# Optimization experiments

Measured on AMD Instinct MI355X. Metric: run time of the kernel, lower is better.

The kernel has to match this reference:

```python
import jax, jax.numpy as jnp
import numpy as np

FEATURE_DIM = 128
HIDDEN_DIM = 64
MAPPING_SIZE = 64
SCALE = 10.0
B, N, H, W = 8, 65536, 56, 56


def setup_inputs() -> dict:
    key = jax.random.key(0)
    ks = jax.random.split(key, 12)
    features = jax.random.normal(ks[0], (B, FEATURE_DIM, H, W), dtype=jnp.float32)
    # points in [-1, 1]^3
    points = jax.random.uniform(ks[1], (B, N, 3), dtype=jnp.float32, minval=-1.0, maxval=1.0)
    # realistic pinhole intrinsics for a 56x56 feature map
    k_mat = jnp.array([[56.0, 0.0, 28.0], [0.0, 56.0, 28.0], [0.0, 0.0, 1.0]], dtype=jnp.float32)
    k = jnp.broadcast_to(k_mat, (B, 3, 3))
    # extrinsics: identity rotation, translate z by 2 so points are in front of camera
    rt_mat = jnp.concatenate([jnp.eye(3, dtype=jnp.float32), jnp.array([[0.0], [0.0], [2.0]], dtype=jnp.float32)], axis=1)
    rt = jnp.broadcast_to(rt_mat, (B, 3, 4))
    # learned params
    B_gauss = jax.random.normal(ks[2], (MAPPING_SIZE, 3), dtype=jnp.float32) * SCALE
    input_dim = FEATURE_DIM + 2 * MAPPING_SIZE
    W1 = jax.random.normal(ks[3], (input_dim, HIDDEN_DIM), dtype=jnp.float32) * 0.05
    b1 = jnp.zeros((HIDDEN_DIM,), dtype=jnp.float32)
    W2 = jax.random.normal(ks[4], (HIDDEN_DIM, HIDDEN_DIM), dtype=jnp.float32) * 0.05
    b2 = jnp.zeros((HIDDEN_DIM,), dtype=jnp.float32)
    W3 = jax.random.normal(ks[5], (HIDDEN_DIM, HIDDEN_DIM), dtype=jnp.float32) * 0.05
    b3 = jnp.zeros((HIDDEN_DIM,), dtype=jnp.float32)
    W4 = jax.random.normal(ks[6], (HIDDEN_DIM, 1), dtype=jnp.float32) * 0.05
    b4 = jnp.zeros((1,), dtype=jnp.float32)
    return {"features": features, "points": points, "k": k, "rt": rt,
            "B_gauss": B_gauss, "W1": W1, "b1": b1, "W2": W2, "b2": b2,
            "W3": W3, "b3": b3, "W4": W4, "b4": b4}


def _grid_sample_bilinear_zeros(grid, x, y):
    # grid: (B, C, H, W); x, y: (B, N) pixel coords (align_corners=False already unnormalized)
    Bc, C, Hc, Wc = grid.shape
    g = jnp.transpose(grid, (0, 2, 3, 1))  # (B, H, W, C)
    x0 = jnp.floor(x)
    y0 = jnp.floor(y)
    wx1 = x - x0  # frac
    wy1 = y - y0
    wx0 = 1.0 - wx1
    wy0 = 1.0 - wy1
    x0i = x0.astype(jnp.int32)
    y0i = y0.astype(jnp.int32)
    bidx = jnp.arange(Bc, dtype=jnp.int32)[:, None]  # (B, 1)

    def gather(ix, iy):
        inb = ((ix >= 0) & (ix < Wc) & (iy >= 0) & (iy < Hc)).astype(grid.dtype)  # (B, N)
        vals = g[bidx, jnp.clip(iy, 0, Hc - 1), jnp.clip(ix, 0, Wc - 1)]  # (B, N, C)
        return vals * inb[..., None]

    out = (gather(x0i, y0i) * (wx0 * wy0)[..., None]
           + gather(x0i + 1, y0i) * (wx1 * wy0)[..., None]
           + gather(x0i, y0i + 1) * (wx0 * wy1)[..., None]
           + gather(x0i + 1, y0i + 1) * (wx1 * wy1)[..., None])
    return out  # (B, N, C)


def reference(features, points, k, rt, B_gauss, W1, b1, W2, b2, W3, b3, W4, b4):
    Bc, Nc, _ = points.shape
    Hc, Wc = features.shape[-2:]
    # --- camera projection ---
    homo = jnp.concatenate([points, jnp.ones((Bc, Nc, 1), dtype=points.dtype)], axis=2)  # (B,N,4)
    cam = jnp.einsum('bij,bnj->bni', rt, homo)   # (B,N,3)
    img = jnp.einsum('bij,bnj->bni', k, cam)     # (B,N,3)
    z = img[:, :, 2:3] + 1e-8
    uv = img[:, :, :2] / z
    valid = (img[:, :, 2:3] > 0).astype(points.dtype)  # (B,N,1)
    u_norm = (2.0 * uv[..., 0] + 1.0) / Wc - 1.0
    v_norm = (2.0 * uv[..., 1] + 1.0) / Hc - 1.0
    # grid_sample align_corners=False unnormalization: ix = ((g+1)*W - 1)/2
    x = ((u_norm + 1.0) * Wc - 1.0) * 0.5
    y = ((v_norm + 1.0) * Hc - 1.0) * 0.5
    img_feats = _grid_sample_bilinear_zeros(features, x, y) * valid  # (B,N,C)
    # --- Fourier mapping ---
    x_proj = (2.0 * np.pi) * jnp.einsum('bnd,md->bnm', points, B_gauss)  # (B,N,M)
    coord_feats = jnp.concatenate([jnp.sin(x_proj), jnp.cos(x_proj)], axis=-1)  # (B,N,2M)
    # --- MLP ---
    inp = jnp.concatenate([img_feats, coord_feats], axis=2)  # (B,N,C+2M)
    h = jax.nn.relu(inp @ W1 + b1)
    h = jax.nn.relu(h @ W2 + b2)
    h = jax.nn.relu(h @ W3 + b3)
    out = h @ W4 + b4  # (B,N,1)
    return out
```

## Files before the change

### kernel.cpp

```cpp
#include <hip/hip_runtime.h>

#define FDIM 128
#define HDIM 64
#define MSIZE 64
#define IMG_W 56
#define IMG_H 56
#define NPIX (IMG_W * IMG_H)
#define NB 8
#define NPTS 65536

typedef _Float16 f16x8 __attribute__((ext_vector_type(8)));
typedef __fp16 hf16x2 __attribute__((ext_vector_type(2)));
typedef float f32x4 __attribute__((ext_vector_type(4)));
typedef int i32x4 __attribute__((ext_vector_type(4)));

#define W2_OFF 16384
#define W3_OFF 20480
#define FT_BYTE_OFF 49152
#define TR16_BLOCKS (NPIX / 16 * NB)

__device__ __forceinline__ void lds_fence() {
    __asm__ volatile("s_waitcnt lgkmcnt(0)" ::: "memory");
}

__global__ __launch_bounds__(256) void prep_kernel(const float* __restrict__ in,
                                                   const float* __restrict__ W1,
                                                   const float* __restrict__ W2,
                                                   const float* __restrict__ W3,
                                                   _Float16* __restrict__ ws) {
    if (blockIdx.x < TR16_BLOCKS) {
        __shared__ float tile[16][133];
        _Float16* out = ws + FT_BYTE_OFF / 2;
        const int b = blockIdx.x / (NPIX / 16);
        const int pbase = (blockIdx.x % (NPIX / 16)) * 16;
        const int t = threadIdx.x;
        const float* src = in + (size_t)b * FDIM * NPIX;
        _Float16*    dst = out + (size_t)b * NPIX * FDIM;
        const int pq = t & 3;
        const int ch = t >> 2;
#pragma unroll
        for (int it = 0; it < 2; ++it) {
            const int c = it * 64 + ch;
            const float4 v = *(const float4*)(src + (size_t)c * NPIX + pbase + pq * 4);
            tile[pq * 4 + 0][c] = v.x;
            tile[pq * 4 + 1][c] = v.y;
            tile[pq * 4 + 2][c] = v.z;
            tile[pq * 4 + 3][c] = v.w;
        }
        __syncthreads();
        const int px = t >> 4;
        const int hk = (t & 15) * 8;
        union { f16x8 v; hf16x2 h[4]; } hv;
#pragma unroll
        for (int j = 0; j < 4; ++j)
            hv.h[j] = __builtin_amdgcn_cvt_pkrtz(tile[px][hk + 2 * j], tile[px][hk + 2 * j + 1]);
        *(f16x8*)(dst + (size_t)(pbase + px) * FDIM + hk) = hv.v;
    } else {
        const int t = (blockIdx.x - TR16_BLOCKS) * 256 + threadIdx.x;
        const int l = t & 63;
        const int q = l >> 4;
        const int col = l & 15;
        const int frag = t >> 6;
        if (frag < 32) {
            const int kt = frag >> 2, nt = frag & 3;
#pragma unroll
            for (int j = 0; j < 8; ++j) {
                int k = kt * 32 + q * 8 + j;
                int row = (k < 128) ? k : (128 + (k & 1) * 64 + ((k - 128) >> 1));
                ws[((size_t)(frag * 64 + l)) * 8 + j] = (_Float16)W1[row * HDIM + nt * 16 + col];
            }
        } else if (frag < 40) {
            const int f2 = frag - 32;
            const int kt = f2 >> 2, nt = f2 & 3;
#pragma unroll
            for (int j = 0; j < 8; ++j) {
                int row = kt * 32 + q * 8 + j;
                ws[W2_OFF + ((size_t)(f2 * 64 + l)) * 8 + j] = (_Float16)W2[row * HDIM + nt * 16 + col];
            }
        } else {
            const int f3 = frag - 40;
            const int kt = f3 >> 2, nt = f3 & 3;
#pragma unroll
            for (int j = 0; j < 8; ++j) {
                int row = kt * 32 + q * 8 + j;
                ws[W3_OFF + ((size_t)(f3 * 64 + l)) * 8 + j] = (_Float16)W3[row * HDIM + nt * 16 + col];
            }
        }
    }
}

__global__ __launch_bounds__(256, 4) void decoder_mfma3(
    const _Float16* __restrict__ ft,
    const float* __restrict__ points,
    const float* __restrict__ Kmat, const float* __restrict__ Rt,
    const float* __restrict__ Bg,
    const _Float16* __restrict__ wfrag,
    const float* __restrict__ b1, const float* __restrict__ b2,
    const float* __restrict__ b3,
    const float* __restrict__ W4, const float* __restrict__ b4,
    float* __restrict__ out) {
    __shared__ _Float16 lds[4 * 32 * 72];
    const int tid = threadIdx.x;
    const int wid = tid >> 6;
    const int l   = tid & 63;
    const int q   = l >> 4;
    const int col = l & 15;
    const int b    = blockIdx.x & 7;
    const int grp  = blockIdx.x >> 3;
    const int base = b * NPTS + grp * 128 + wid * 32;
    _Float16* Ah = lds + wid * 32 * 72;
    float* sh = (float*)Ah;
    int*   shi = (int*)Ah;

    if (l < 32) {
        const int gid = base + l;
        const float px = points[(size_t)gid * 3 + 0];
        const float py = points[(size_t)gid * 3 + 1];
        const float pz = points[(size_t)gid * 3 + 2];
        const float* rt = Rt + b * 12;
        const float* km = Kmat + b * 9;
        float cx = rt[0] * px + rt[1] * py + rt[2]  * pz + rt[3];
        float cy = rt[4] * px + rt[5] * py + rt[6]  * pz + rt[7];
        float cz = rt[8] * px + rt[9] * py + rt[10] * pz + rt[11];
        float ix = km[0] * cx + km[1] * cy + km[2] * cz;
        float iy = km[3] * cx + km[4] * cy + km[5] * cz;
        float iz = km[6] * cx + km[7] * cy + km[8] * cz;
        float z  = iz + 1e-8f;
        float u  = ix / z;
        float v  = iy / z;
        float valid = (iz > 0.0f) ? 1.0f : 0.0f;
        float u_norm = (2.0f * u + 1.0f) / (float)IMG_W - 1.0f;
        float v_norm = (2.0f * v + 1.0f) / (float)IMG_H - 1.0f;
        float x = ((u_norm + 1.0f) * (float)IMG_W - 1.0f) * 0.5f;
        float y = ((v_norm + 1.0f) * (float)IMG_H - 1.0f) * 0.5f;
        float x0f = floorf(x), y0f = floorf(y);
        float wx1 = x - x0f, wy1 = y - y0f;
        float wx0 = 1.0f - wx1, wy0 = 1.0f - wy1;
        int x0 = (int)x0f, y0 = (int)y0f;
        int x1 = x0 + 1, y1 = y0 + 1;
        int x0c = x0 < 0 ? 0 : (x0 > IMG_W - 1 ? IMG_W - 1 : x0);
        int x1c = x1 < 0 ? 0 : (x1 > IMG_W - 1 ? IMG_W - 1 : x1);
        int y0c = y0 < 0 ? 0 : (y0 > IMG_H - 1 ? IMG_H - 1 : y0);
        int y1c = y1 < 0 ? 0 : (y1 > IMG_H - 1 ? IMG_H - 1 : y1);
        float mx0 = (x0 >= 0 && x0 < IMG_W) ? 1.0f : 0.0f;
        float mx1 = (x1 >= 0 && x1 < IMG_W) ? 1.0f : 0.0f;
        float my0 = (y0 >= 0 && y0 < IMG_H) ? 1.0f : 0.0f;
        float my1 = (y1 >= 0 && y1 < IMG_H) ? 1.0f : 0.0f;
        const int pb = b * NPIX;
        sh[l * 12 + 0] = wx0 * wy0 * mx0 * my0 * valid;
        sh[l * 12 + 1] = wx1 * wy0 * mx1 * my0 * valid;
        sh[l * 12 + 2] = wx0 * wy1 * mx0 * my1 * valid;
        sh[l * 12 + 3] = wx1 * wy1 * mx1 * my1 * valid;
        shi[l * 12 + 4] = (pb + y0c * IMG_W + x0c) * FDIM;
        shi[l * 12 + 5] = (pb + y0c * IMG_W + x1c) * FDIM;
        shi[l * 12 + 6] = (pb + y1c * IMG_W + x0c) * FDIM;
        shi[l * 12 + 7] = (pb + y1c * IMG_W + x1c) * FDIM;
        sh[l * 12 + 8]  = px;
        sh[l * 12 + 9]  = py;
        sh[l * 12 + 10] = pz;
    }
    lds_fence();

    const f32x4 zero4 = {0.0f, 0.0f, 0.0f, 0.0f};
    f32x4 acc[2][4];
#pragma unroll
    for (int mt = 0; mt < 2; ++mt)
#pragma unroll
        for (int nt = 0; nt < 4; ++nt) acc[mt][nt] = zero4;

    f32x4 wv[2];
    i32x4 iv[2];
    float qx[2], qy[2], qz[2];
#pragma unroll
    for (int mt = 0; mt < 2; ++mt) {
        const float* e = sh + (mt * 16 + col) * 12;
        wv[mt] = *(const f32x4*)(e);
        iv[mt] = *(const i32x4*)(e + 4);
        qx[mt] = e[8]; qy[mt] = e[9]; qz[mt] = e[10];
    }

    f16x8 c00 = *(const f16x8*)(ft + iv[0].x + q * 8);
    f16x8 c10 = *(const f16x8*)(ft + iv[0].y + q * 8);
    f16x8 c01 = *(const f16x8*)(ft + iv[0].z + q * 8);
    f16x8 c11 = *(const f16x8*)(ft + iv[0].w + q * 8);

#pragma unroll
    for (int ktf = 0; ktf < 4; ++ktf) {
        float bgx[4], bgy[4], bgz[4];
#pragma unroll
        for (int i = 0; i < 4; ++i) {
            const int m = ktf * 16 + q * 4 + i;
            bgx[i] = Bg[m * 3 + 0];
            bgy[i] = Bg[m * 3 + 1];
            bgz[i] = Bg[m * 3 + 2];
        }
        f16x8 bf[4];
#pragma unroll
        for (int nt = 0; nt < 4; ++nt)
            bf[nt] = *(const f16x8*)(wfrag + ((size_t)(((4 + ktf) * 4 + nt) * 64 + l)) * 8);
#pragma unroll
        for (int mt = 0; mt < 2; ++mt) {
            union { f16x8 v; hf16x2 h[4]; } af;
#pragma unroll
            for (int i = 0; i < 4; ++i) {
                float t = bgx[i] * qx[mt] + bgy[i] * qy[mt] + bgz[i] * qz[mt];
                float tf = __builtin_amdgcn_fractf(t);
                af.h[i] = __builtin_amdgcn_cvt_pkrtz(__builtin_amdgcn_sinf(tf),
                                                     __builtin_amdgcn_cosf(tf));
            }
#pragma unroll
            for (int nt = 0; nt < 4; ++nt)
                acc[mt][nt] = __builtin_amdgcn_mfma_f32_16x16x32_f16(af.v, bf[nt], acc[mt][nt], 0, 0, 0);
        }
    }

    _Float16 wh[2][4];
#pragma unroll
    for (int mt = 0; mt < 2; ++mt) {
        wh[mt][0] = (_Float16)wv[mt].x; wh[mt][1] = (_Float16)wv[mt].y;
        wh[mt][2] = (_Float16)wv[mt].z; wh[mt][3] = (_Float16)wv[mt].w;
    }
#pragma unroll
    for (int s = 0; s < 8; ++s) {
        const int mt = s >> 2, ktg = s & 3;
        f16x8 n00, n10, n01, n11;
        if (s < 7) {
            const int nmt = (s + 1) >> 2, nktg = (s + 1) & 3;
            const int co = nktg * 32 + q * 8;
            n00 = *(const f16x8*)(ft + iv[nmt].x + co);
            n10 = *(const f16x8*)(ft + iv[nmt].y + co);
            n01 = *(const f16x8*)(ft + iv[nmt].z + co);
            n11 = *(const f16x8*)(ft + iv[nmt].w + co);
        }
        f16x8 af = c00 * wh[mt][0] + c10 * wh[mt][1] + c01 * wh[mt][2] + c11 * wh[mt][3];
#pragma unroll
        for (int nt = 0; nt < 4; ++nt) {
            f16x8 bf = *(const f16x8*)(wfrag + ((size_t)((ktg * 4 + nt) * 64 + l)) * 8);
            acc[mt][nt] = __builtin_amdgcn_mfma_f32_16x16x32_f16(af, bf, acc[mt][nt], 0, 0, 0);
        }
        c00 = n00; c10 = n10; c01 = n01; c11 = n11;
    }

    float bb[4];
#pragma unroll
    for (int nt = 0; nt < 4; ++nt) bb[nt] = b1[nt * 16 + col];
#pragma unroll
    for (int mt = 0; mt < 2; ++mt)
#pragma unroll
        for (int nt = 0; nt < 4; ++nt)
#pragma unroll
            for (int r = 0; r < 4; ++r) {
                float hv = fmaxf(acc[mt][nt][r] + bb[nt], 0.0f);
                Ah[(mt * 16 + q * 4 + r) * 72 + nt * 16 + col] = (_Float16)hv;
            }
    lds_fence();

#pragma unroll
    for (int mt = 0; mt < 2; ++mt)
#pragma unroll
        for (int nt = 0; nt < 4; ++nt) acc[mt][nt] = zero4;
#pragma unroll
    for (int ktl = 0; ktl < 2; ++ktl) {
        f16x8 bf[4];
#pragma unroll
        for (int nt = 0; nt < 4; ++nt)
            bf[nt] = *(const f16x8*)(wfrag + W2_OFF + ((size_t)((ktl * 4 + nt) * 64 + l)) * 8);
#pragma unroll
        for (int mt = 0; mt < 2; ++mt) {
            f16x8 af = *(const f16x8*)(&Ah[(mt * 16 + col) * 72 + ktl * 32 + q * 8]);
#pragma unroll
            for (int nt = 0; nt < 4; ++nt)
                acc[mt][nt] = __builtin_amdgcn_mfma_f32_16x16x32_f16(af, bf[nt], acc[mt][nt], 0, 0, 0);
        }
    }
    lds_fence();
#pragma unroll
    for (int nt = 0; nt < 4; ++nt) bb[nt] = b2[nt * 16 + col];
#pragma unroll
    for (int mt = 0; mt < 2; ++mt)
#pragma unroll
        for (int nt = 0; nt < 4; ++nt)
#pragma unroll
            for (int r = 0; r < 4; ++r) {
                float hv = fmaxf(acc[mt][nt][r] + bb[nt], 0.0f);
                Ah[(mt * 16 + q * 4 + r) * 72 + nt * 16 + col] = (_Float16)hv;
            }
    lds_fence();

#pragma unroll
    for (int mt = 0; mt < 2; ++mt)
#pragma unroll
        for (int nt = 0; nt < 4; ++nt) acc[mt][nt] = zero4;
#pragma unroll
    for (int ktl = 0; ktl < 2; ++ktl) {
        f16x8 bf[4];
#pragma unroll
        for (int nt = 0; nt < 4; ++nt)
            bf[nt] = *(const f16x8*)(wfrag + W3_OFF + ((size_t)((ktl * 4 + nt) * 64 + l)) * 8);
#pragma unroll
        for (int mt = 0; mt < 2; ++mt) {
            f16x8 af = *(const f16x8*)(&Ah[(mt * 16 + col) * 72 + ktl * 32 + q * 8]);
#pragma unroll
            for (int nt = 0; nt < 4; ++nt)
                acc[mt][nt] = __builtin_amdgcn_mfma_f32_16x16x32_f16(af, bf[nt], acc[mt][nt], 0, 0, 0);
        }
    }

    float b3v[4], w4v[4];
#pragma unroll
    for (int nt = 0; nt < 4; ++nt) {
        b3v[nt] = b3[nt * 16 + col];
        w4v[nt] = W4[nt * 16 + col];
    }
    const float b4v = b4[0];
#pragma unroll
    for (int mt = 0; mt < 2; ++mt)
#pragma unroll
        for (int r = 0; r < 4; ++r) {
            float p = 0.0f;
#pragma unroll
            for (int nt = 0; nt < 4; ++nt)
                p = fmaf(fmaxf(acc[mt][nt][r] + b3v[nt], 0.0f), w4v[nt], p);
            p += __shfl_xor(p, 1);
            p += __shfl_xor(p, 2);
            p += __shfl_xor(p, 4);
            p += __shfl_xor(p, 8);
            if (col == 0) out[base + mt * 16 + q * 4 + r] = p + b4v;
        }
}

__global__ __launch_bounds__(64, 2) void decoder_valu(
    const float* __restrict__ feats, const float* __restrict__ points,
    const float* __restrict__ Kmat, const float* __restrict__ Rt,
    const float* __restrict__ Bg,
    const float* __restrict__ W1, const float* __restrict__ b1,
    const float* __restrict__ W2, const float* __restrict__ b2,
    const float* __restrict__ W3, const float* __restrict__ b3,
    const float* __restrict__ W4, const float* __restrict__ b4,
    float* __restrict__ out) {
    __shared__ float hbuf[64 * 65];
    const int tid = threadIdx.x;
    const int b   = blockIdx.x / (NPTS / 64);
    const int gid = blockIdx.x * 64 + tid;
    const float px = points[(size_t)gid * 3 + 0];
    const float py = points[(size_t)gid * 3 + 1];
    const float pz = points[(size_t)gid * 3 + 2];
    const float* rt = Rt + b * 12;
    const float* km = Kmat + b * 9;
    float cx = rt[0] * px + rt[1] * py + rt[2]  * pz + rt[3];
    float cy = rt[4] * px + rt[5] * py + rt[6]  * pz + rt[7];
    float cz = rt[8] * px + rt[9] * py + rt[10] * pz + rt[11];
    float ix = km[0] * cx + km[1] * cy + km[2] * cz;
    float iy = km[3] * cx + km[4] * cy + km[5] * cz;
    float iz = km[6] * cx + km[7] * cy + km[8] * cz;
    float z  = iz + 1e-8f;
    float u  = ix / z, v = iy / z;
    float valid = (iz > 0.0f) ? 1.0f : 0.0f;
    float u_norm = (2.0f * u + 1.0f) / (float)IMG_W - 1.0f;
    float v_norm = (2.0f * v + 1.0f) / (float)IMG_H - 1.0f;
    float x = ((u_norm + 1.0f) * (float)IMG_W - 1.0f) * 0.5f;
    float y = ((v_norm + 1.0f) * (float)IMG_H - 1.0f) * 0.5f;
    float x0f = floorf(x), y0f = floorf(y);
    float wx1 = x - x0f, wy1 = y - y0f;
    float wx0 = 1.0f - wx1, wy0 = 1.0f - wy1;
    int x0 = (int)x0f, y0 = (int)y0f;
    int x1 = x0 + 1, y1 = y0 + 1;
    int x0c = x0 < 0 ? 0 : (x0 > IMG_W - 1 ? IMG_W - 1 : x0);
    int x1c = x1 < 0 ? 0 : (x1 > IMG_W - 1 ? IMG_W - 1 : x1);
    int y0c = y0 < 0 ? 0 : (y0 > IMG_H - 1 ? IMG_H - 1 : y0);
    int y1c = y1 < 0 ? 0 : (y1 > IMG_H - 1 ? IMG_H - 1 : y1);
    float mx0 = (x0 >= 0 && x0 < IMG_W) ? 1.0f : 0.0f;
    float mx1 = (x1 >= 0 && x1 < IMG_W) ? 1.0f : 0.0f;
    float my0 = (y0 >= 0 && y0 < IMG_H) ? 1.0f : 0.0f;
    float my1 = (y1 >= 0 && y1 < IMG_H) ? 1.0f : 0.0f;
    float w00 = wx0 * wy0 * mx0 * my0 * valid;
    float w10 = wx1 * wy0 * mx1 * my0 * valid;
    float w01 = wx0 * wy1 * mx0 * my1 * valid;
    float w11 = wx1 * wy1 * mx1 * my1 * valid;
    float h[HDIM];
#pragma unroll
    for (int j = 0; j < HDIM; ++j) h[j] = b1[j];
    const float* fb = feats + (size_t)b * FDIM * NPIX;
    const int p00 = y0c * IMG_W + x0c, p10 = y0c * IMG_W + x1c;
    const int p01 = y1c * IMG_W + x0c, p11 = y1c * IMG_W + x1c;
#pragma unroll 1
    for (int c = 0; c < FDIM; ++c) {
        const float* fp = fb + (size_t)c * NPIX;
        float fv = w00 * fp[p00] + w10 * fp[p10] + w01 * fp[p01] + w11 * fp[p11];
        const float* wr = W1 + (size_t)c * HDIM;
#pragma unroll
        for (int j = 0; j < HDIM; ++j) h[j] = fmaf(fv, wr[j], h[j]);
    }
#pragma unroll 1
    for (int m = 0; m < MSIZE; ++m) {
        float t = Bg[m * 3 + 0] * px + Bg[m * 3 + 1] * py + Bg[m * 3 + 2] * pz;
        float tf = t - floorf(t);
        float s = __builtin_amdgcn_sinf(tf);
        float c = __builtin_amdgcn_cosf(tf);
        const float* wsn = W1 + (size_t)(FDIM + m) * HDIM;
        const float* wcs = W1 + (size_t)(FDIM + MSIZE + m) * HDIM;
#pragma unroll
        for (int j = 0; j < HDIM; ++j)
            h[j] = fmaf(s, wsn[j], fmaf(c, wcs[j], h[j]));
    }
    float* myh = &hbuf[tid * 65];
#pragma unroll
    for (int j = 0; j < HDIM; ++j) myh[j] = fmaxf(h[j], 0.0f);
    float h2[HDIM];
#pragma unroll
    for (int j = 0; j < HDIM; ++j) h2[j] = b2[j];
#pragma unroll 1
    for (int i = 0; i < HDIM; ++i) {
        float hi = myh[i];
        const float* wr = W2 + (size_t)i * HDIM;
#pragma unroll
        for (int j = 0; j < HDIM; ++j) h2[j] = fmaf(hi, wr[j], h2[j]);
    }
#pragma unroll
    for (int j = 0; j < HDIM; ++j) myh[j] = fmaxf(h2[j], 0.0f);
#pragma unroll
    for (int j = 0; j < HDIM; ++j) h[j] = b3[j];
#pragma unroll 1
    for (int i = 0; i < HDIM; ++i) {
        float hi = myh[i];
        const float* wr = W3 + (size_t)i * HDIM;
#pragma unroll
        for (int j = 0; j < HDIM; ++j) h[j] = fmaf(hi, wr[j], h[j]);
    }
    float acc = b4[0];
#pragma unroll
    for (int j = 0; j < HDIM; ++j) acc = fmaf(fmaxf(h[j], 0.0f), W4[j], acc);
    out[gid] = acc;
}

extern "C" void kernel_launch(void* const* d_in, const int* in_sizes, int n_in,
                              void* d_out, int out_size, void* d_ws, size_t ws_size,
                              hipStream_t stream) {
    const float* feats = (const float*)d_in[0];
    const float* pts   = (const float*)d_in[1];
    const float* k     = (const float*)d_in[2];
    const float* rt    = (const float*)d_in[3];
    const float* Bg    = (const float*)d_in[4];
    const float* W1    = (const float*)d_in[5];
    const float* b1    = (const float*)d_in[6];
    const float* W2    = (const float*)d_in[7];
    const float* b2    = (const float*)d_in[8];
    const float* W3    = (const float*)d_in[9];
    const float* b3    = (const float*)d_in[10];
    const float* W4    = (const float*)d_in[11];
    const float* b4    = (const float*)d_in[12];
    float* out = (float*)d_out;

    const size_t ftBytes = (size_t)NB * NPIX * FDIM * sizeof(_Float16);

    if (ws_size >= FT_BYTE_OFF + ftBytes) {
        _Float16* wf = (_Float16*)d_ws;
        _Float16* ft = (_Float16*)((char*)d_ws + FT_BYTE_OFF);
        prep_kernel<<<TR16_BLOCKS + 12, 256, 0, stream>>>(feats, W1, W2, W3, wf);
        decoder_mfma3<<<NB * NPTS / 128, 256, 0, stream>>>(ft, pts, k, rt, Bg, wf,
                                                           b1, b2, b3, W4, b4, out);
    } else {
        decoder_valu<<<NB * NPTS / 64, 64, 0, stream>>>(feats, pts, k, rt, Bg,
                                                        W1, b1, W2, b2, W3, b3, W4, b4, out);
    }
}
```

Before: 182.3 us.

## Fuse prep and decoder into one persistent kernel with per-batch spin barrier

Merges the feature transpose/fp16 conversion, weight fragment packing and MLP decoder into one kernel of 1024 blocks. Each block transposes a slice of its batch's feature map, then waits on per-batch atomic counters (plus a weight counter) before processing four point groups in a loop. This removes a second kernel launch and the global gap between prep and decode, and lets decoding of one batch start as soon as that batch's features are ready. In exchange it relies on all 1024 blocks being co-resident, since the spin wait would deadlock otherwise, and adds a memset and atomic polling.

New measurement: 538.4 us. +195.3%, slower.

```diff
diff --git a/kernel.cpp b/kernel.cpp
--- a/kernel.cpp
+++ b/kernel.cpp
@@ -16,47 +16,33 @@
 
 #define W2_OFF 16384
 #define W3_OFF 20480
-#define FT_BYTE_OFF 49152
-#define TR16_BLOCKS (NPIX / 16 * NB)
+#define CNT_OFF 49152
+#define FT_BYTE_OFF 49664
 
 __device__ __forceinline__ void lds_fence() {
     __asm__ volatile("s_waitcnt lgkmcnt(0)" ::: "memory");
 }
 
-__global__ __launch_bounds__(256) void prep_kernel(const float* __restrict__ in,
-                                                   const float* __restrict__ W1,
-                                                   const float* __restrict__ W2,
-                                                   const float* __restrict__ W3,
-                                                   _Float16* __restrict__ ws) {
-    if (blockIdx.x < TR16_BLOCKS) {
-        __shared__ float tile[16][133];
-        _Float16* out = ws + FT_BYTE_OFF / 2;
-        const int b = blockIdx.x / (NPIX / 16);
-        const int pbase = (blockIdx.x % (NPIX / 16)) * 16;
-        const int t = threadIdx.x;
-        const float* src = in + (size_t)b * FDIM * NPIX;
-        _Float16*    dst = out + (size_t)b * NPIX * FDIM;
-        const int pq = t & 3;
-        const int ch = t >> 2;
-#pragma unroll
-        for (int it = 0; it < 2; ++it) {
-            const int c = it * 64 + ch;
-            const float4 v = *(const float4*)(src + (size_t)c * NPIX + pbase + pq * 4);
-            tile[pq * 4 + 0][c] = v.x;
-            tile[pq * 4 + 1][c] = v.y;
-            tile[pq * 4 + 2][c] = v.z;
-            tile[pq * 4 + 3][c] = v.w;
-        }
-        __syncthreads();
-        const int px = t >> 4;
-        const int hk = (t & 15) * 8;
-        union { f16x8 v; hf16x2 h[4]; } hv;
-#pragma unroll
-        for (int j = 0; j < 4; ++j)
-            hv.h[j] = __builtin_amdgcn_cvt_pkrtz(tile[px][hk + 2 * j], tile[px][hk + 2 * j + 1]);
-        *(f16x8*)(dst + (size_t)(pbase + px) * FDIM + hk) = hv.v;
-    } else {
-        const int t = (blockIdx.x - TR16_BLOCKS) * 256 + threadIdx.x;
+__global__ __launch_bounds__(256, 4) void fused_all(
+    const float* __restrict__ feats, const float* __restrict__ points,
+    const float* __restrict__ Kmat, const float* __restrict__ Rt,
+    const float* __restrict__ Bg,
+    const float* __restrict__ W1, const float* __restrict__ W2,
+    const float* __restrict__ W3,
+    const float* __restrict__ b1, const float* __restrict__ b2,
+    const float* __restrict__ b3,
+    const float* __restrict__ W4, const float* __restrict__ b4,
+    _Float16* __restrict__ ws, float* __restrict__ out) {
+    __shared__ __align__(16) char smem[4 * 32 * 72 * 2];
+    int* cnt = (int*)((char*)ws + CNT_OFF);
+    _Float16* ft = (_Float16*)((char*)ws + FT_BYTE_OFF);
+    const int g   = blockIdx.x;
+    const int tid = threadIdx.x;
+    const int b   = g & 7;
+    const int sub = g >> 3;
+
+    if (g < 12) {
+        const int t = g * 256 + tid;
         const int l = t & 63;
         const int q = l >> 4;
         const int col = l & 15;
@@ -87,246 +73,281 @@
             }
         }
     }
-}
-
-__global__ __launch_bounds__(256, 4) void decoder_mfma3(
-    const _Float16* __restrict__ ft,
-    const float* __restrict__ points,
-    const float* __restrict__ Kmat, const float* __restrict__ Rt,
-    const float* __restrict__ Bg,
-    const _Float16* __restrict__ wfrag,
-    const float* __restrict__ b1, const float* __restrict__ b2,
-    const float* __restrict__ b3,
-    const float* __restrict__ W4, const float* __restrict__ b4,
-    float* __restrict__ out) {
-    __shared__ _Float16 lds[4 * 32 * 72];
-    const int tid = threadIdx.x;
+
+    if (sub < 49) {
+        float (*tile)[133] = (float (*)[133])smem;
+        const float* src = feats + (size_t)b * FDIM * NPIX;
+        _Float16*    dst = ft + (size_t)b * NPIX * FDIM;
+        const int pq = tid & 3;
+        const int ch = tid >> 2;
+        const int px = tid >> 4;
+        const int hk = (tid & 15) * 8;
+#pragma unroll 1
+        for (int st = 0; st < 4; ++st) {
+            const int pbase = sub * 64 + st * 16;
+            __syncthreads();
+#pragma unroll
+            for (int it = 0; it < 2; ++it) {
+                const int c = it * 64 + ch;
+                const float4 v = *(const float4*)(src + (size_t)c * NPIX + pbase + pq * 4);
+                tile[pq * 4 + 0][c] = v.x;
+                tile[pq * 4 + 1][c] = v.y;
+                tile[pq * 4 + 2][c] = v.z;
+                tile[pq * 4 + 3][c] = v.w;
+            }
+            __syncthreads();
+            union { f16x8 v; hf16x2 h[4]; } hv;
+#pragma unroll
+            for (int j = 0; j < 4; ++j)
+                hv.h[j] = __builtin_amdgcn_cvt_pkrtz(tile[px][hk + 2 * j], tile[px][hk + 2 * j + 1]);
+            *(f16x8*)(dst + (size_t)(pbase + px) * FDIM + hk) = hv.v;
+        }
+    }
+
+    __syncthreads();
+    __threadfence();
+    if (tid == 0) {
+        atomicAdd(&cnt[b], 1);
+        if (g < 12) atomicAdd(&cnt[8], 1);
+    }
+    if (tid == 0) {
+        while (atomicAdd(&cnt[b], 0) < 128 || atomicAdd(&cnt[8], 0) < 12)
+            __builtin_amdgcn_s_sleep(2);
+    }
+    __syncthreads();
+    __threadfence();
+
+    const _Float16* wfrag = ws;
     const int wid = tid >> 6;
     const int l   = tid & 63;
     const int q   = l >> 4;
     const int col = l & 15;
-    const int b    = blockIdx.x & 7;
-    const int grp  = blockIdx.x >> 3;
-    const int base = b * NPTS + grp * 128 + wid * 32;
-    _Float16* Ah = lds + wid * 32 * 72;
+    _Float16* Ah = (_Float16*)smem + wid * 32 * 72;
     float* sh = (float*)Ah;
     int*   shi = (int*)Ah;
-
-    if (l < 32) {
-        const int gid = base + l;
-        const float px = points[(size_t)gid * 3 + 0];
-        const float py = points[(size_t)gid * 3 + 1];
-        const float pz = points[(size_t)gid * 3 + 2];
-        const float* rt = Rt + b * 12;
-        const float* km = Kmat + b * 9;
-        float cx = rt[0] * px + rt[1] * py + rt[2]  * pz + rt[3];
-        float cy = rt[4] * px + rt[5] * py + rt[6]  * pz + rt[7];
-        float cz = rt[8] * px + rt[9] * py + rt[10] * pz + rt[11];
-        float ix = km[0] * cx + km[1] * cy + km[2] * cz;
-        float iy = km[3] * cx + km[4] * cy + km[5] * cz;
-        float iz = km[6] * cx + km[7] * cy + km[8] * cz;
-        float z  = iz + 1e-8f;
-        float u  = ix / z;
-        float v  = iy / z;
-        float valid = (iz > 0.0f) ? 1.0f : 0.0f;
-        float u_norm = (2.0f * u + 1.0f) / (float)IMG_W - 1.0f;
-        float v_norm = (2.0f * v + 1.0f) / (float)IMG_H - 1.0f;
-        float x = ((u_norm + 1.0f) * (float)IMG_W - 1.0f) * 0.5f;
-        float y = ((v_norm + 1.0f) * (float)IMG_H - 1.0f) * 0.5f;
-        float x0f = floorf(x), y0f = floorf(y);
-        float wx1 = x - x0f, wy1 = y - y0f;
-        float wx0 = 1.0f - wx1, wy0 = 1.0f - wy1;
-        int x0 = (int)x0f, y0 = (int)y0f;
-        int x1 = x0 + 1, y1 = y0 + 1;
-        int x0c = x0 < 0 ? 0 : (x0 > IMG_W - 1 ? IMG_W - 1 : x0);
-        int x1c = x1 < 0 ? 0 : (x1 > IMG_W - 1 ? IMG_W - 1 : x1);
-        int y0c = y0 < 0 ? 0 : (y0 > IMG_H - 1 ? IMG_H - 1 : y0);
-        int y1c = y1 < 0 ? 0 : (y1 > IMG_H - 1 ? IMG_H - 1 : y1);
-        float mx0 = (x0 >= 0 && x0 < IMG_W) ? 1.0f : 0.0f;
-        float mx1 = (x1 >= 0 && x1 < IMG_W) ? 1.0f : 0.0f;
-        float my0 = (y0 >= 0 && y0 < IMG_H) ? 1.0f : 0.0f;
-        float my1 = (y1 >= 0 && y1 < IMG_H) ? 1.0f : 0.0f;
-        const int pb = b * NPIX;
-        sh[l * 12 + 0] = wx0 * wy0 * mx0 * my0 * valid;
-        sh[l * 12 + 1] = wx1 * wy0 * mx1 * my0 * valid;
-        sh[l * 12 + 2] = wx0 * wy1 * mx0 * my1 * valid;
-        sh[l * 12 + 3] = wx1 * wy1 * mx1 * my1 * valid;
-        shi[l * 12 + 4] = (pb + y0c * IMG_W + x0c) * FDIM;
-        shi[l * 12 + 5] = (pb + y0c * IMG_W + x1c) * FDIM;
-        shi[l * 12 + 6] = (pb + y1c * IMG_W + x0c) * FDIM;
-        shi[l * 12 + 7] = (pb + y1c * IMG_W + x1c) * FDIM;
-        sh[l * 12 + 8]  = px;
-        sh[l * 12 + 9]  = py;
-        sh[l * 12 + 10] = pz;
-    }
-    lds_fence();
-
     const f32x4 zero4 = {0.0f, 0.0f, 0.0f, 0.0f};
-    f32x4 acc[2][4];
-#pragma unroll
-    for (int mt = 0; mt < 2; ++mt)
-#pragma unroll
-        for (int nt = 0; nt < 4; ++nt) acc[mt][nt] = zero4;
-
-    f32x4 wv[2];
-    i32x4 iv[2];
-    float qx[2], qy[2], qz[2];
-#pragma unroll
-    for (int mt = 0; mt < 2; ++mt) {
-        const float* e = sh + (mt * 16 + col) * 12;
-        wv[mt] = *(const f32x4*)(e);
-        iv[mt] = *(const i32x4*)(e + 4);
-        qx[mt] = e[8]; qy[mt] = e[9]; qz[mt] = e[10];
-    }
-
-    f16x8 c00 = *(const f16x8*)(ft + iv[0].x + q * 8);
-    f16x8 c10 = *(const f16x8*)(ft + iv[0].y + q * 8);
-    f16x8 c01 = *(const f16x8*)(ft + iv[0].z + q * 8);
-    f16x8 c11 = *(const f16x8*)(ft + iv[0].w + q * 8);
-
-#pragma unroll
-    for (int ktf = 0; ktf < 4; ++ktf) {
-        float bgx[4], bgy[4], bgz[4];
-#pragma unroll
-        for (int i = 0; i < 4; ++i) {
-            const int m = ktf * 16 + q * 4 + i;
-            bgx[i] = Bg[m * 3 + 0];
-            bgy[i] = Bg[m * 3 + 1];
-            bgz[i] = Bg[m * 3 + 2];
-        }
-        f16x8 bf[4];
-#pragma unroll
-        for (int nt = 0; nt < 4; ++nt)
-            bf[nt] = *(const f16x8*)(wfrag + ((size_t)(((4 + ktf) * 4 + nt) * 64 + l)) * 8);
+
+#pragma unroll 1
+    for (int iter = 0; iter < 4; ++iter) {
+        const int grp  = sub * 4 + iter;
+        const int base = b * NPTS + grp * 128 + wid * 32;
+        lds_fence();
+
+        if (l < 32) {
+            const int gid = base + l;
+            const float px = points[(size_t)gid * 3 + 0];
+            const float py = points[(size_t)gid * 3 + 1];
+            const float pz = points[(size_t)gid * 3 + 2];
+            const float* rt = Rt + b * 12;
+            const float* km = Kmat + b * 9;
+            float cx = rt[0] * px + rt[1] * py + rt[2]  * pz + rt[3];
+            float cy = rt[4] * px + rt[5] * py + rt[6]  * pz + rt[7];
+            float cz = rt[8] * px + rt[9] * py + rt[10] * pz + rt[11];
+            float ix = km[0] * cx + km[1] * cy + km[2] * cz;
+            float iy = km[3] * cx + km[4] * cy + km[5] * cz;
+            float iz = km[6] * cx + km[7] * cy + km[8] * cz;
+            float z  = iz + 1e-8f;
+            float u  = ix / z;
+            float v  = iy / z;
+            float valid = (iz > 0.0f) ? 1.0f : 0.0f;
+            float u_norm = (2.0f * u + 1.0f) / (float)IMG_W - 1.0f;
+            float v_norm = (2.0f * v + 1.0f) / (float)IMG_H - 1.0f;
+            float x = ((u_norm + 1.0f) * (float)IMG_W - 1.0f) * 0.5f;
+            float y = ((v_norm + 1.0f) * (float)IMG_H - 1.0f) * 0.5f;
+            float x0f = floorf(x), y0f = floorf(y);
+            float wx1 = x - x0f, wy1 = y - y0f;
+            float wx0 = 1.0f - wx1, wy0 = 1.0f - wy1;
+            int x0 = (int)x0f, y0 = (int)y0f;
+            int x1 = x0 + 1, y1 = y0 + 1;
+            int x0c = x0 < 0 ? 0 : (x0 > IMG_W - 1 ? IMG_W - 1 : x0);
+            int x1c = x1 < 0 ? 0 : (x1 > IMG_W - 1 ? IMG_W - 1 : x1);
+            int y0c = y0 < 0 ? 0 : (y0 > IMG_H - 1 ? IMG_H - 1 : y0);
+            int y1c = y1 < 0 ? 0 : (y1 > IMG_H - 1 ? IMG_H - 1 : y1);
+            float mx0 = (x0 >= 0 && x0 < IMG_W) ? 1.0f : 0.0f;
+            float mx1 = (x1 >= 0 && x1 < IMG_W) ? 1.0f : 0.0f;
+            float my0 = (y0 >= 0 && y0 < IMG_H) ? 1.0f : 0.0f;
+            float my1 = (y1 >= 0 && y1 < IMG_H) ? 1.0f : 0.0f;
+            const int pb = b * NPIX;
+            sh[l * 12 + 0] = wx0 * wy0 * mx0 * my0 * valid;
+            sh[l * 12 + 1] = wx1 * wy0 * mx1 * my0 * valid;
+            sh[l * 12 + 2] = wx0 * wy1 * mx0 * my1 * valid;
+            sh[l * 12 + 3] = wx1 * wy1 * mx1 * my1 * valid;
+            shi[l * 12 + 4] = (pb + y0c * IMG_W + x0c) * FDIM;
+            shi[l * 12 + 5] = (pb + y0c * IMG_W + x1c) * FDIM;
+            shi[l * 12 + 6] = (pb + y1c * IMG_W + x0c) * FDIM;
+            shi[l * 12 + 7] = (pb + y1c * IMG_W + x1c) * FDIM;
+            sh[l * 12 + 8]  = px;
+            sh[l * 12 + 9]  = py;
+            sh[l * 12 + 10] = pz;
+        }
+        lds_fence();
+
+        f32x4 acc[2][4];
+#pragma unroll
+        for (int mt = 0; mt < 2; ++mt)
+#pragma unroll
+            for (int nt = 0; nt < 4; ++nt) acc[mt][nt] = zero4;
+
+        f32x4 wv[2];
+        i32x4 iv[2];
+        float qx[2], qy[2], qz[2];
 #pragma unroll
         for (int mt = 0; mt < 2; ++mt) {
-            union { f16x8 v; hf16x2 h[4]; } af;
+            const float* e = sh + (mt * 16 + col) * 12;
+            wv[mt] = *(const f32x4*)(e);
+            iv[mt] = *(const i32x4*)(e + 4);
+            qx[mt] = e[8]; qy[mt] = e[9]; qz[mt] = e[10];
+        }
+
+        f16x8 c00 = *(const f16x8*)(ft + iv[0].x + q * 8);
+        f16x8 c10 = *(const f16x8*)(ft + iv[0].y + q * 8);
+        f16x8 c01 = *(const f16x8*)(ft + iv[0].z + q * 8);
+        f16x8 c11 = *(const f16x8*)(ft + iv[0].w + q * 8);
+
+#pragma unroll
+        for (int ktf = 0; ktf < 4; ++ktf) {
+            float bgx[4], bgy[4], bgz[4];
 #pragma unroll
             for (int i = 0; i < 4; ++i) {
-                float t = bgx[i] * qx[mt] + bgy[i] * qy[mt] + bgz[i] * qz[mt];
-                float tf = __builtin_amdgcn_fractf(t);
-                af.h[i] = __builtin_amdgcn_cvt_pkrtz(__builtin_amdgcn_sinf(tf),
-                                                     __builtin_amdgcn_cosf(tf));
-            }
+                const int m = ktf * 16 + q * 4 + i;
+                bgx[i] = Bg[m * 3 + 0];
+                bgy[i] = Bg[m * 3 + 1];
+                bgz[i] = Bg[m * 3 + 2];
+            }
+            f16x8 bf[4];
 #pragma unroll
             for (int nt = 0; nt < 4; ++nt)
-                acc[mt][nt] = __builtin_amdgcn_mfma_f32_16x16x32_f16(af.v, bf[nt], acc[mt][nt], 0, 0, 0);
-        }
-    }
-
-    _Float16 wh[2][4];
-#pragma unroll
-    for (int mt = 0; mt < 2; ++mt) {
-        wh[mt][0] = (_Float16)wv[mt].x; wh[mt][1] = (_Float16)wv[mt].y;
-        wh[mt][2] = (_Float16)wv[mt].z; wh[mt][3] = (_Float16)wv[mt].w;
-    }
-#pragma unroll
-    for (int s = 0; s < 8; ++s) {
-        const int mt = s >> 2, ktg = s & 3;
-        f16x8 n00, n10, n01, n11;
-        if (s < 7) {
-            const int nmt = (s + 1) >> 2, nktg = (s + 1) & 3;
-            const int co = nktg * 32 + q * 8;
-            n00 = *(const f16x8*)(ft + iv[nmt].x + co);
-            n10 = *(const f16x8*)(ft + iv[nmt].y + co);
-            n01 = *(const f16x8*)(ft + iv[nmt].z + co);
-            n11 = *(const f16x8*)(ft + iv[nmt].w + co);
-        }
-        f16x8 af = c00 * wh[mt][0] + c10 * wh[mt][1] + c01 * wh[mt][2] + c11 * wh[mt][3];
+                bf[nt] = *(const f16x8*)(wfrag + ((size_t)(((4 + ktf) * 4 + nt) * 64 + l)) * 8);
+#pragma unroll
+            for (int mt = 0; mt < 2; ++mt) {
+                union { f16x8 v; hf16x2 h[4]; } af;
+#pragma unroll
+                for (int i = 0; i < 4; ++i) {
+                    float t = bgx[i] * qx[mt] + bgy[i] * qy[mt] + bgz[i] * qz[mt];
+                    float tf = __builtin_amdgcn_fractf(t);
+                    af.h[i] = __builtin_amdgcn_cvt_pkrtz(__builtin_amdgcn_sinf(tf),
+                                                         __builtin_amdgcn_cosf(tf));
+                }
+#pragma unroll
+                for (int nt = 0; nt < 4; ++nt)
+                    acc[mt][nt] = __builtin_amdgcn_mfma_f32_16x16x32_f16(af.v, bf[nt], acc[mt][nt], 0, 0, 0);
+            }
+        }
+
+        _Float16 wh[2][4];
+#pragma unroll
+        for (int mt = 0; mt < 2; ++mt) {
+            wh[mt][0] = (_Float16)wv[mt].x; wh[mt][1] = (_Float16)wv[mt].y;
+            wh[mt][2] = (_Float16)wv[mt].z; wh[mt][3] = (_Float16)wv[mt].w;
+        }
+#pragma unroll
+        for (int s = 0; s < 8; ++s) {
+            const int mt = s >> 2, ktg = s & 3;
+            f16x8 n00, n10, n01, n11;
+            if (s < 7) {
+                const int nmt = (s + 1) >> 2, nktg = (s + 1) & 3;
+                const int co = nktg * 32 + q * 8;
+                n00 = *(const f16x8*)(ft + iv[nmt].x + co);
+                n10 = *(const f16x8*)(ft + iv[nmt].y + co);
+                n01 = *(const f16x8*)(ft + iv[nmt].z + co);
+                n11 = *(const f16x8*)(ft + iv[nmt].w + co);
+            }
+            f16x8 af = c00 * wh[mt][0] + c10 * wh[mt][1] + c01 * wh[mt][2] + c11 * wh[mt][3];
+#pragma unroll
+            for (int nt = 0; nt < 4; ++nt) {
+                f16x8 bf = *(const f16x8*)(wfrag + ((size_t)((ktg * 4 + nt) * 64 + l)) * 8);
+                acc[mt][nt] = __builtin_amdgcn_mfma_f32_16x16x32_f16(af, bf, acc[mt][nt], 0, 0, 0);
+            }
+            c00 = n00; c10 = n10; c01 = n01; c11 = n11;
+        }
+
+        float bb[4];
+#pragma unroll
+        for (int nt = 0; nt < 4; ++nt) bb[nt] = b1[nt * 16 + col];
+#pragma unroll
+        for (int mt = 0; mt < 2; ++mt)
+#pragma unroll
+            for (int nt = 0; nt < 4; ++nt)
+#pragma unroll
+                for (int r = 0; r < 4; ++r) {
+                    float hv = fmaxf(acc[mt][nt][r] + bb[nt], 0.0f);
+                    Ah[(mt * 16 + q * 4 + r) * 72 + nt * 16 + col] = (_Float16)hv;
+                }
+        lds_fence();
+
+#pragma unroll
+        for (int mt = 0; mt < 2; ++mt)
+#pragma unroll
+            for (int nt = 0; nt < 4; ++nt) acc[mt][nt] = zero4;
+#pragma unroll
+        for (int ktl = 0; ktl < 2; ++ktl) {
+            f16x8 bf[4];
+#pragma unroll
+            for (int nt = 0; nt < 4; ++nt)
+                bf[nt] = *(const f16x8*)(wfrag + W2_OFF + ((size_t)((ktl * 4 + nt) * 64 + l)) * 8);
+#pragma unroll
+            for (int mt = 0; mt < 2; ++mt) {
+                f16x8 af = *(const f16x8*)(&Ah[(mt * 16 + col) * 72 + ktl * 32 + q * 8]);
+#pragma unroll
+                for (int nt = 0; nt < 4; ++nt)
+                    acc[mt][nt] = __builtin_amdgcn_mfma_f32_16x16x32_f16(af, bf[nt], acc[mt][nt], 0, 0, 0);
+            }
+        }
+        lds_fence();
+#pragma unroll
+        for (int nt = 0; nt < 4; ++nt) bb[nt] = b2[nt * 16 + col];
+#pragma unroll
+        for (int mt = 0; mt < 2; ++mt)
+#pragma unroll
+            for (int nt = 0; nt < 4; ++nt)
+#pragma unroll
+                for (int r = 0; r < 4; ++r) {
+                    float hv = fmaxf(acc[mt][nt][r] + bb[nt], 0.0f);
+                    Ah[(mt * 16 + q * 4 + r) * 72 + nt * 16 + col] = (_Float16)hv;
+                }
+        lds_fence();
+
+#pragma unroll
+        for (int mt = 0; mt < 2; ++mt)
+#pragma unroll
+            for (int nt = 0; nt < 4; ++nt) acc[mt][nt] = zero4;
+#pragma unroll
+        for (int ktl = 0; ktl < 2; ++ktl) {
+            f16x8 bf[4];
+#pragma unroll
+            for (int nt = 0; nt < 4; ++nt)
+                bf[nt] = *(const f16x8*)(wfrag + W3_OFF + ((size_t)((ktl * 4 + nt) * 64 + l)) * 8);
+#pragma unroll
+            for (int mt = 0; mt < 2; ++mt) {
+                f16x8 af = *(const f16x8*)(&Ah[(mt * 16 + col) * 72 + ktl * 32 + q * 8]);
+#pragma unroll
+                for (int nt = 0; nt < 4; ++nt)
+                    acc[mt][nt] = __builtin_amdgcn_mfma_f32_16x16x32_f16(af, bf[nt], acc[mt][nt], 0, 0, 0);
+            }
+        }
+
+        float b3v[4], w4v[4];
 #pragma unroll
         for (int nt = 0; nt < 4; ++nt) {
-            f16x8 bf = *(const f16x8*)(wfrag + ((size_t)((ktg * 4 + nt) * 64 + l)) * 8);
-            acc[mt][nt] = __builtin_amdgcn_mfma_f32_16x16x32_f16(af, bf, acc[mt][nt], 0, 0, 0);
-        }
-        c00 = n00; c10 = n10; c01 = n01; c11 = n11;
-    }
-
-    float bb[4];
-#pragma unroll
-    for (int nt = 0; nt < 4; ++nt) bb[nt] = b1[nt * 16 + col];
-#pragma unroll
-    for (int mt = 0; mt < 2; ++mt)
-#pragma unroll
-        for (int nt = 0; nt < 4; ++nt)
+            b3v[nt] = b3[nt * 16 + col];
+            w4v[nt] = W4[nt * 16 + col];
+        }
+        const float b4v = b4[0];
+#pragma unroll
+        for (int mt = 0; mt < 2; ++mt)
 #pragma unroll
             for (int r = 0; r < 4; ++r) {
-                float hv = fmaxf(acc[mt][nt][r] + bb[nt], 0.0f);
-                Ah[(mt * 16 + q * 4 + r) * 72 + nt * 16 + col] = (_Float16)hv;
-            }
-    lds_fence();
-
-#pragma unroll
-    for (int mt = 0; mt < 2; ++mt)
-#pragma unroll
-        for (int nt = 0; nt < 4; ++nt) acc[mt][nt] = zero4;
-#pragma unroll
-    for (int ktl = 0; ktl < 2; ++ktl) {
-        f16x8 bf[4];
-#pragma unroll
-        for (int nt = 0; nt < 4; ++nt)
-            bf[nt] = *(const f16x8*)(wfrag + W2_OFF + ((size_t)((ktl * 4 + nt) * 64 + l)) * 8);
-#pragma unroll
-        for (int mt = 0; mt < 2; ++mt) {
-            f16x8 af = *(const f16x8*)(&Ah[(mt * 16 + col) * 72 + ktl * 32 + q * 8]);
-#pragma unroll
-            for (int nt = 0; nt < 4; ++nt)
-                acc[mt][nt] = __builtin_amdgcn_mfma_f32_16x16x32_f16(af, bf[nt], acc[mt][nt], 0, 0, 0);
-        }
-    }
-    lds_fence();
-#pragma unroll
-    for (int nt = 0; nt < 4; ++nt) bb[nt] = b2[nt * 16 + col];
-#pragma unroll
-    for (int mt = 0; mt < 2; ++mt)
-#pragma unroll
-        for (int nt = 0; nt < 4; ++nt)
-#pragma unroll
-            for (int r = 0; r < 4; ++r) {
-                float hv = fmaxf(acc[mt][nt][r] + bb[nt], 0.0f);
-                Ah[(mt * 16 + q * 4 + r) * 72 + nt * 16 + col] = (_Float16)hv;
-            }
-    lds_fence();
-
-#pragma unroll
-    for (int mt = 0; mt < 2; ++mt)
-#pragma unroll
-        for (int nt = 0; nt < 4; ++nt) acc[mt][nt] = zero4;
-#pragma unroll
-    for (int ktl = 0; ktl < 2; ++ktl) {
-        f16x8 bf[4];
-#pragma unroll
-        for (int nt = 0; nt < 4; ++nt)
-            bf[nt] = *(const f16x8*)(wfrag + W3_OFF + ((size_t)((ktl * 4 + nt) * 64 + l)) * 8);
-#pragma unroll
-        for (int mt = 0; mt < 2; ++mt) {
-            f16x8 af = *(const f16x8*)(&Ah[(mt * 16 + col) * 72 + ktl * 32 + q * 8]);
-#pragma unroll
-            for (int nt = 0; nt < 4; ++nt)
-                acc[mt][nt] = __builtin_amdgcn_mfma_f32_16x16x32_f16(af, bf[nt], acc[mt][nt], 0, 0, 0);
-        }
-    }
-
-    float b3v[4], w4v[4];
-#pragma unroll
-    for (int nt = 0; nt < 4; ++nt) {
-        b3v[nt] = b3[nt * 16 + col];
-        w4v[nt] = W4[nt * 16 + col];
-    }
-    const float b4v = b4[0];
-#pragma unroll
-    for (int mt = 0; mt < 2; ++mt)
-#pragma unroll
-        for (int r = 0; r < 4; ++r) {
-            float p = 0.0f;
-#pragma unroll
-            for (int nt = 0; nt < 4; ++nt)
-                p = fmaf(fmaxf(acc[mt][nt][r] + b3v[nt], 0.0f), w4v[nt], p);
-            p += __shfl_xor(p, 1);
-            p += __shfl_xor(p, 2);
-            p += __shfl_xor(p, 4);
-            p += __shfl_xor(p, 8);
-            if (col == 0) out[base + mt * 16 + q * 4 + r] = p + b4v;
-        }
+                float p = 0.0f;
+#pragma unroll
+                for (int nt = 0; nt < 4; ++nt)
+                    p = fmaf(fmaxf(acc[mt][nt][r] + b3v[nt], 0.0f), w4v[nt], p);
+                p += __shfl_xor(p, 1);
+                p += __shfl_xor(p, 2);
+                p += __shfl_xor(p, 4);
+                p += __shfl_xor(p, 8);
+                if (col == 0) out[base + mt * 16 + q * 4 + r] = p + b4v;
+            }
+    }
 }
 
 __global__ __launch_bounds__(64, 2) void decoder_valu(
@@ -455,10 +476,9 @@
 
     if (ws_size >= FT_BYTE_OFF + ftBytes) {
         _Float16* wf = (_Float16*)d_ws;
-        _Float16* ft = (_Float16*)((char*)d_ws + FT_BYTE_OFF);
-        prep_kernel<<<TR16_BLOCKS + 12, 256, 0, stream>>>(feats, W1, W2, W3, wf);
-        decoder_mfma3<<<NB * NPTS / 128, 256, 0, stream>>>(ft, pts, k, rt, Bg, wf,
-                                                           b1, b2, b3, W4, b4, out);
+        hipMemsetAsync((char*)d_ws + CNT_OFF, 0, 64, stream);
+        fused_all<<<1024, 256, 0, stream>>>(feats, pts, k, rt, Bg, W1, W2, W3,
+                                            b1, b2, b3, W4, b4, wf, out);
     } else {
         decoder_valu<<<NB * NPTS / 64, 64, 0, stream>>>(feats, pts, k, rt, Bg,
                                                         W1, b1, W2, b2, W3, b3, W4, b4, out);
```
